# Performance work log

Measured on AMD Instinct MI355X. Metric: run time of the kernel, lower is better.

Reference implementation:

```python
import jax, jax.numpy as jnp
import numpy as np

NUM_USERS = 200000
NUM_ITEMS = 100000
EMB = 64
NUM_LAYERS = 3


def setup_inputs() -> dict:
    rng = np.random.default_rng(0)
    E_INTER = 2_000_000
    # unique (user, item) interactions -> faithful to adj[e0, e1] = 1.0 set-semantics
    lin = np.unique(rng.integers(0, NUM_USERS * NUM_ITEMS, size=E_INTER, dtype=np.int64))
    u = (lin // NUM_ITEMS).astype(np.int32)
    it = (lin % NUM_ITEMS).astype(np.int32) + NUM_USERS  # item node ids offset by NUM_USERS
    row = np.concatenate([u, it])  # symmetric bipartite graph, no self-loops
    col = np.concatenate([it, u])
    edge_index = jnp.asarray(np.stack([row, col]), dtype=jnp.int32)  # [2, E]

    key = jax.random.key(0)
    k1, k2 = jax.random.split(key)
    # xavier_uniform on nn.Embedding.weight
    bu = float(np.sqrt(6.0 / (NUM_USERS + EMB)))
    bi = float(np.sqrt(6.0 / (NUM_ITEMS + EMB)))
    user_emb = jax.random.uniform(k1, (NUM_USERS, EMB), jnp.float32, -bu, bu)
    item_emb = jax.random.uniform(k2, (NUM_ITEMS, EMB), jnp.float32, -bi, bi)
    return {"edge_index": edge_index, "user_emb": user_emb, "item_emb": item_emb}


def reference(edge_index, user_emb, item_emb):
    num_users = user_emb.shape[0]
    N = num_users + item_emb.shape[0]
    x = jnp.concatenate([user_emb, item_emb], axis=0)  # ego embeddings [N, D]
    row, col = edge_index[0], edge_index[1]

    # adj has unique off-diagonal edges + eye(N): row-sum degree = edge count + 1
    deg = jax.ops.segment_sum(jnp.ones(row.shape, x.dtype), row, num_segments=N) + 1.0
    dinv = jax.lax.rsqrt(deg)                 # deg >= 1, never inf
    w = (dinv[row] * dinv[col])[:, None]      # per-edge D^-1/2 A D^-1/2 weight
    self_w = (dinv * dinv)[:, None]           # self-loop weight d_i^-1

    acc = x  # sum over layer outputs, including layer 0
    for _ in range(NUM_LAYERS):
        x = jax.ops.segment_sum(w * x[col], row, num_segments=N) + self_w * x
        # dropout is identity in eval mode
        acc = acc + x

    return acc[:num_users], acc[num_users:]
```

## Files before the change

kernel.cpp:

```cpp
#include <hip/hip_runtime.h>
#include <hip/hip_bf16.h>

#define EMB 64

__device__ __forceinline__ float bf2f(unsigned short h) {
    return __uint_as_float(((unsigned)h) << 16);
}
__device__ __forceinline__ unsigned short f2bf(float f) {
    unsigned u = __float_as_uint(f);
    unsigned r = (u + 0x7fffu + ((u >> 16) & 1u)) >> 16;
    return (unsigned short)r;
}

__global__ void k1_kernel(const int* __restrict__ row, const int* __restrict__ colh,
                          int* __restrict__ urp, int* __restrict__ degit,
                          int NU, int Eh, int urp_blocks) {
    if ((int)blockIdx.x < urp_blocks) {
        int r = blockIdx.x * blockDim.x + threadIdx.x;
        if (r > NU) return;
        if (r == NU) { urp[NU] = Eh; return; }
        int lo = 0, hi = Eh;
        while (lo < hi) {
            int mid = (lo + hi) >> 1;
            if (row[mid] < r) lo = mid + 1; else hi = mid;
        }
        urp[r] = lo;
    } else {
        int e = (blockIdx.x - urp_blocks) * blockDim.x + threadIdx.x;
        if (e < Eh) atomicAdd(&degit[colh[e] - NU], 1);
    }
}

__global__ void k3_kernel(const int* __restrict__ degit, int* __restrict__ excl,
                          int* __restrict__ partials,
                          const int* __restrict__ urp, float* __restrict__ dinv,
                          const float* __restrict__ ue, const float* __restrict__ ie,
                          unsigned short* __restrict__ y0,
                          int NU, int NI, int N, long nu_elems, long total,
                          int nb_s1, int nb_dv) {
    int b = blockIdx.x;
    if (b < nb_s1) {
        __shared__ int sh[256];
        int t = threadIdx.x;
        int base = b * 1024 + t * 4;
        int d0 = (base + 0 < NI) ? degit[base + 0] : 0;
        int d1 = (base + 1 < NI) ? degit[base + 1] : 0;
        int d2 = (base + 2 < NI) ? degit[base + 2] : 0;
        int d3 = (base + 3 < NI) ? degit[base + 3] : 0;
        int tsum = d0 + d1 + d2 + d3;
        sh[t] = tsum;
        __syncthreads();
        for (int off = 1; off < 256; off <<= 1) {
            int v = (t >= off) ? sh[t - off] : 0;
            __syncthreads();
            sh[t] += v;
            __syncthreads();
        }
        int excl_t = sh[t] - tsum;
        if (base + 0 < NI) excl[base + 0] = excl_t;
        if (base + 1 < NI) excl[base + 1] = excl_t + d0;
        if (base + 2 < NI) excl[base + 2] = excl_t + d0 + d1;
        if (base + 3 < NI) excl[base + 3] = excl_t + d0 + d1 + d2;
        if (t == 255) partials[b] = sh[t];
    } else if (b < nb_s1 + nb_dv) {
        int i = (b - nb_s1) * blockDim.x + threadIdx.x;
        if (i >= N) return;
        int d = (i < NU) ? (urp[i + 1] - urp[i]) : degit[i - NU];
        dinv[i] = rsqrtf((float)d + 1.0f);
    } else {
        long j4 = ((long)(b - nb_s1 - nb_dv) * blockDim.x + threadIdx.x) * 4;
        if (j4 >= total) return;
        int node = (int)(j4 >> 6);
        int d = (node < NU) ? (urp[node + 1] - urp[node]) : degit[node - NU];
        float sc = rsqrtf((float)d + 1.0f);
        float4 v = (j4 < nu_elems) ? ((const float4*)ue)[j4 >> 2]
                                   : ((const float4*)ie)[(j4 - nu_elems) >> 2];
        ushort4 o;
        o.x = f2bf(sc * v.x); o.y = f2bf(sc * v.y);
        o.z = f2bf(sc * v.z); o.w = f2bf(sc * v.w);
        ((ushort4*)y0)[j4 >> 2] = o;
    }
}

__global__ void scan2_kernel(int* __restrict__ partials, int nb) {
    __shared__ int sh[512];
    int t = threadIdx.x;
    int v = (t < nb) ? partials[t] : 0;
    sh[t] = v;
    __syncthreads();
    for (int off = 1; off < 512; off <<= 1) {
        int u = (t >= off) ? sh[t - off] : 0;
        __syncthreads();
        sh[t] += u;
        __syncthreads();
    }
    if (t < nb) partials[t] = sh[t] - v;
}

__global__ void scan3_kernel(const int* __restrict__ excl, const int* __restrict__ partials,
                             int* __restrict__ irp, int* __restrict__ cursor, int NI, int Eh) {
    int i = blockIdx.x * blockDim.x + threadIdx.x;
    if (i < NI) {
        int v = excl[i] + partials[i >> 10];
        irp[i] = v;
        cursor[i] = v;
    }
    if (i == NI) irp[NI] = Eh;
}

__device__ __forceinline__ void spmm_node(
    int i, int q,
    const int* __restrict__ urp, const int* __restrict__ irp,
    const int* __restrict__ colg, const int* __restrict__ icols,
    const float* __restrict__ dinv,
    const unsigned short* __restrict__ yc,
    unsigned short* __restrict__ yn,
    const unsigned short* __restrict__ y0b,
    const unsigned short* __restrict__ y1b,
    float* __restrict__ out, int NU) {
    const int* list;
    int s, e;
    if (i < NU) { s = urp[i]; e = urp[i + 1]; list = colg; }
    else        { int j = i - NU; s = irp[j]; e = irp[j + 1]; list = icols; }
    float di = dinv[i];
    const ushort4* __restrict__ yc4 = (const ushort4*)yc;

    long p = (long)i * 16 + q;
    ushort4 sv = yc4[p];

    float ax = 0.f, ay = 0.f, az = 0.f, aw = 0.f;
    for (int k0 = s; k0 < e; k0 += 8) {
        int   c[8];
        float w[8];
#pragma unroll
        for (int j = 0; j < 8; ++j) {
            int k = k0 + j;
            bool v = (k < e);
            c[j] = v ? list[k] : 0;
            w[j] = v ? 1.0f : 0.0f;
        }
        ushort4 u[8];
#pragma unroll
        for (int j = 0; j < 8; ++j) u[j] = yc4[(long)c[j] * 16 + q];
#pragma unroll
        for (int j = 0; j < 8; ++j) {
            ax += w[j] * bf2f(u[j].x);
            ay += w[j] * bf2f(u[j].y);
            az += w[j] * bf2f(u[j].z);
            aw += w[j] * bf2f(u[j].w);
        }
    }

    ax += bf2f(sv.x);
    ay += bf2f(sv.y);
    az += bf2f(sv.z);
    aw += bf2f(sv.w);

    if (yn) {
        float t = di * di;
        ushort4 o;
        o.x = f2bf(t * ax); o.y = f2bf(t * ay); o.z = f2bf(t * az); o.w = f2bf(t * aw);
        ((ushort4*)yn)[p] = o;
    } else {
        ushort4 a0 = ((const ushort4*)y0b)[p];
        ushort4 a1 = ((const ushort4*)y1b)[p];
        float inv = 1.0f / di;
        float4 o;
        o.x = (bf2f(a0.x) + bf2f(a1.x) + bf2f(sv.x)) * inv + di * ax;
        o.y = (bf2f(a0.y) + bf2f(a1.y) + bf2f(sv.y)) * inv + di * ay;
        o.z = (bf2f(a0.z) + bf2f(a1.z) + bf2f(sv.z)) * inv + di * az;
        o.w = (bf2f(a0.w) + bf2f(a1.w) + bf2f(sv.w)) * inv + di * aw;
        ((float4*)out)[p] = o;
    }
}

__global__ void spmm_kernel(int base, int cnt,
                            const int* __restrict__ urp, const int* __restrict__ irp,
                            const int* __restrict__ colg, const int* __restrict__ icols,
                            const float* __restrict__ dinv,
                            const unsigned short* __restrict__ yc,
                            unsigned short* __restrict__ yn,
                            const unsigned short* __restrict__ y0b,
                            const unsigned short* __restrict__ y1b,
                            float* __restrict__ out, int NU) {
    long t = (long)blockIdx.x * blockDim.x + threadIdx.x;
    int r = (int)(t >> 4);
    if (r >= cnt) return;
    spmm_node(base + r, (int)(t & 15), urp, irp, colg, icols, dinv,
              yc, yn, y0b, y1b, out, NU);
}

__global__ void m6_kernel(const int* __restrict__ rowh, const int* __restrict__ colh,
                          int* __restrict__ cursor, int* __restrict__ icols,
                          int nb_if, int Eh, int NU, int NI,
                          const int* __restrict__ urp, const int* __restrict__ irp,
                          const int* __restrict__ colg,
                          const float* __restrict__ dinv,
                          const unsigned short* __restrict__ yc,
                          unsigned short* __restrict__ yn) {
    int b = (int)blockIdx.x;
    int fid = -1, usr;
    if (b < 4 * nb_if) {
        if ((b & 3) == 0) { fid = b >> 2; usr = -1; }
        else              { usr = b - (b >> 2) - 1; }
    } else {
        usr = b - nb_if;
    }

    if (fid >= 0) {
        int t = threadIdx.x;
        long cb = (long)fid * 1024;
        int c[4], u[4];
#pragma unroll
        for (int j = 0; j < 4; ++j) {
            long e = cb + j * 256 + t;
            bool v = (e < Eh);
            c[j] = v ? (colh[e] - NU) : -1;
            u[j] = v ? rowh[e] : 0;
        }
        int slice = (NI + 7) >> 3;
        for (int p = 0; p < 8; ++p) {
            int lo = p * slice, hi = lo + slice;
#pragma unroll
            for (int j = 0; j < 4; ++j) {
                if (c[j] >= lo && c[j] < hi) {
                    int pos = atomicAdd(&cursor[c[j]], 1);
                    icols[pos] = u[j];
                }
            }
        }
    } else {
        long t = (long)usr * blockDim.x + threadIdx.x;
        int i = (int)(t >> 4);
        if (i >= NU) return;
        spmm_node(i, (int)(t & 15), urp, irp, colg, nullptr, dinv,
                  yc, yn, nullptr, nullptr, nullptr, NU);
    }
}

extern "C" void kernel_launch(void* const* d_in, const int* in_sizes, int n_in,
                              void* d_out, int out_size, void* d_ws, size_t ws_size,
                              hipStream_t stream) {
    const int*   edge_index = (const int*)d_in[0];
    const float* user_emb   = (const float*)d_in[1];
    const float* item_emb   = (const float*)d_in[2];
    float* out = (float*)d_out;

    const int  E  = in_sizes[0] / 2;
    const int  Eh = E / 2;
    const int  NU = in_sizes[1] / EMB;
    const int  NI = in_sizes[2] / EMB;
    const int  N  = NU + NI;
    const long total = (long)N * EMB;

    const int* row = edge_index;
    const int* col = edge_index + E;
    const int* rowh = row;
    const int* colh = col;

    int*   urp      = (int*)d_ws;
    int*   degit    = urp + (NU + 1);
    int*   excl     = degit + NI;
    int*   partials = excl + NI;
    int*   irp      = partials + 512;
    int*   cursor   = irp + (NI + 1);
    int*   icols    = cursor + NI;
    float* dinv     = (float*)(icols + Eh);
    unsigned short* y0 = (unsigned short*)(dinv + N);
    y0 = (unsigned short*)(((uintptr_t)y0 + 15) & ~(uintptr_t)15);
    unsigned short* y1 = y0 + total;
    unsigned short* y2 = y1 + total;

    hipMemsetAsync(degit, 0, (size_t)NI * sizeof(int), stream);

    int urp_blocks  = (NU + 256) / 256;
    int ideg_blocks = (Eh + 255) / 256;
    k1_kernel<<<urp_blocks + ideg_blocks, 256, 0, stream>>>(row, colh, urp, degit,
                                                            NU, Eh, urp_blocks);

    int nb_s1 = (NI + 1023) / 1024;
    int nb_dv = (N + 255) / 256;
    int nb_in = (int)((total / 4 + 255) / 256);
    k3_kernel<<<nb_s1 + nb_dv + nb_in, 256, 0, stream>>>(degit, excl, partials,
                                                         urp, dinv, user_emb, item_emb, y0,
                                                         NU, NI, N, (long)NU * EMB, total,
                                                         nb_s1, nb_dv);

    scan2_kernel<<<1, 512, 0, stream>>>(partials, nb_s1);
    scan3_kernel<<<(NI + 1 + 255) / 256, 256, 0, stream>>>(excl, partials, irp, cursor,
                                                           NI, Eh);

    int nb_if = (Eh + 1023) / 1024;
    int nb_us = (int)(((long)NU * 16 + 255) / 256);
    m6_kernel<<<nb_if + nb_us, 256, 0, stream>>>(rowh, colh, cursor, icols,
                                                 nb_if, Eh, NU, NI,
                                                 urp, irp, col, dinv, y0, y1);

    int nb_it = (int)(((long)NI * 16 + 255) / 256);
    spmm_kernel<<<nb_it, 256, 0, stream>>>(NU, NI, urp, irp, col, icols, dinv,
                                           y0, y1, nullptr, nullptr, nullptr, NU);

    int nb_all = (int)(((long)N * 16 + 255) / 256);
    spmm_kernel<<<nb_all, 256, 0, stream>>>(0, N, urp, irp, col, icols, dinv,
                                            y1, y2, nullptr, nullptr, nullptr, NU);

    spmm_kernel<<<nb_all, 256, 0, stream>>>(0, N, urp, irp, col, icols, dinv,
                                            y2, nullptr, y0, y1, out, NU);
}
```

Measured before the change: 617.6 us.

## Build item CSR via two-pass bucketed counting sort through staging buffer

Replaces the direct scattered atomic insertion of item adjacency lists with a two-pass bucket sort. A first pass groups edges by 1024-item bucket using shared-memory counters and packs the local item offset and user id into one word in a staging buffer. A second pass, fused with the first user-layer SpMM, scatters within each bucket so the cursor atomics and icols writes stay localized. This adds an extra kernel launch and a round trip through staging memory, which aliases the item half of y1 before that half is written.

Result: no change. 624.1 us (+1.0%).

```diff
diff --git a/kernel.cpp b/kernel.cpp
--- a/kernel.cpp
+++ b/kernel.cpp
@@ -2,6 +2,10 @@
 #include <hip/hip_bf16.h>
 
 #define EMB 64
+#define BKT_BITS 10
+#define BKT_SZ   (1 << BKT_BITS)
+#define U_BITS   18
+#define U_MASK   ((1u << U_BITS) - 1u)
 
 __device__ __forceinline__ float bf2f(unsigned short h) {
     return __uint_as_float(((unsigned)h) << 16);
@@ -98,14 +102,49 @@
 }
 
 __global__ void scan3_kernel(const int* __restrict__ excl, const int* __restrict__ partials,
-                             int* __restrict__ irp, int* __restrict__ cursor, int NI, int Eh) {
+                             int* __restrict__ irp, int* __restrict__ cursor,
+                             int* __restrict__ bcur, int NI, int Eh) {
     int i = blockIdx.x * blockDim.x + threadIdx.x;
     if (i < NI) {
         int v = excl[i] + partials[i >> 10];
         irp[i] = v;
         cursor[i] = v;
+        if ((i & (BKT_SZ - 1)) == 0) bcur[i >> BKT_BITS] = v;
     }
     if (i == NI) irp[NI] = Eh;
+}
+
+__global__ void passA_kernel(const int* __restrict__ rowh, const int* __restrict__ colh,
+                             int* __restrict__ bcur, unsigned* __restrict__ staging,
+                             int Eh, int NU, int NB) {
+    __shared__ int cnt[512];
+    __shared__ int base[512];
+    int t = threadIdx.x;
+    for (int j = t; j < NB; j += 256) cnt[j] = 0;
+    __syncthreads();
+    long cb = (long)blockIdx.x * 1024;
+    int b[4], rk[4];
+    unsigned pk[4];
+#pragma unroll
+    for (int j = 0; j < 4; ++j) {
+        long e = cb + j * 256 + t;
+        if (e < Eh) {
+            int u = rowh[e];
+            int loc = colh[e] - NU;
+            b[j] = loc >> BKT_BITS;
+            pk[j] = ((unsigned)(loc & (BKT_SZ - 1)) << U_BITS) | (unsigned)u;
+            rk[j] = atomicAdd(&cnt[b[j]], 1);
+        } else {
+            b[j] = -1;
+        }
+    }
+    __syncthreads();
+    for (int j = t; j < NB; j += 256)
+        base[j] = cnt[j] ? atomicAdd(&bcur[j], cnt[j]) : 0;
+    __syncthreads();
+#pragma unroll
+    for (int j = 0; j < 4; ++j)
+        if (b[j] >= 0) staging[base[b[j]] + rk[j]] = pk[j];
 }
 
 __device__ __forceinline__ void spmm_node(
@@ -190,47 +229,28 @@
               yc, yn, y0b, y1b, out, NU);
 }
 
-__global__ void m6_kernel(const int* __restrict__ rowh, const int* __restrict__ colh,
-                          int* __restrict__ cursor, int* __restrict__ icols,
-                          int nb_if, int Eh, int NU, int NI,
-                          const int* __restrict__ urp, const int* __restrict__ irp,
+__global__ void m6_kernel(const unsigned* __restrict__ staging,
+                          const int* __restrict__ irp, int* __restrict__ cursor,
+                          int* __restrict__ icols, int NB, int NI,
+                          const int* __restrict__ urp,
                           const int* __restrict__ colg,
                           const float* __restrict__ dinv,
                           const unsigned short* __restrict__ yc,
-                          unsigned short* __restrict__ yn) {
+                          unsigned short* __restrict__ yn, int NU) {
     int b = (int)blockIdx.x;
-    int fid = -1, usr;
-    if (b < 4 * nb_if) {
-        if ((b & 3) == 0) { fid = b >> 2; usr = -1; }
-        else              { usr = b - (b >> 2) - 1; }
+    if (b < NB) {
+        int lo = b << BKT_BITS;
+        int hi = lo + BKT_SZ; if (hi > NI) hi = NI;
+        int start = irp[lo], end = irp[hi];
+        for (int k = start + (int)threadIdx.x; k < end; k += 256) {
+            unsigned v = staging[k];
+            int u   = (int)(v & U_MASK);
+            int loc = lo + (int)(v >> U_BITS);
+            int pos = atomicAdd(&cursor[loc], 1);
+            icols[pos] = u;
+        }
     } else {
-        usr = b - nb_if;
-    }
-
-    if (fid >= 0) {
-        int t = threadIdx.x;
-        long cb = (long)fid * 1024;
-        int c[4], u[4];
-#pragma unroll
-        for (int j = 0; j < 4; ++j) {
-            long e = cb + j * 256 + t;
-            bool v = (e < Eh);
-            c[j] = v ? (colh[e] - NU) : -1;
-            u[j] = v ? rowh[e] : 0;
-        }
-        int slice = (NI + 7) >> 3;
-        for (int p = 0; p < 8; ++p) {
-            int lo = p * slice, hi = lo + slice;
-#pragma unroll
-            for (int j = 0; j < 4; ++j) {
-                if (c[j] >= lo && c[j] < hi) {
-                    int pos = atomicAdd(&cursor[c[j]], 1);
-                    icols[pos] = u[j];
-                }
-            }
-        }
-    } else {
-        long t = (long)usr * blockDim.x + threadIdx.x;
+        long t = (long)(b - NB) * blockDim.x + threadIdx.x;
         int i = (int)(t >> 4);
         if (i >= NU) return;
         spmm_node(i, (int)(t & 15), urp, irp, colg, nullptr, dinv,
@@ -262,14 +282,15 @@
     int*   degit    = urp + (NU + 1);
     int*   excl     = degit + NI;
     int*   partials = excl + NI;
-    int*   irp      = partials + 512;
+    int*   bcur     = partials + 512;
+    int*   irp      = bcur + 512;
     int*   cursor   = irp + (NI + 1);
     int*   icols    = cursor + NI;
     float* dinv     = (float*)(icols + Eh);
-    unsigned short* y0 = (unsigned short*)(dinv + N);
-    y0 = (unsigned short*)(((uintptr_t)y0 + 15) & ~(uintptr_t)15);
+    unsigned short* y0 = (unsigned short*)(((uintptr_t)(dinv + N) + 127) & ~(uintptr_t)127);
     unsigned short* y1 = y0 + total;
     unsigned short* y2 = y1 + total;
+    unsigned* staging = (unsigned*)(y1 + (long)NU * EMB);
 
     hipMemsetAsync(degit, 0, (size_t)NI * sizeof(int), stream);
 
@@ -288,13 +309,15 @@
 
     scan2_kernel<<<1, 512, 0, stream>>>(partials, nb_s1);
     scan3_kernel<<<(NI + 1 + 255) / 256, 256, 0, stream>>>(excl, partials, irp, cursor,
-                                                           NI, Eh);
-
-    int nb_if = (Eh + 1023) / 1024;
+                                                           bcur, NI, Eh);
+
+    int NB = (NI + BKT_SZ - 1) >> BKT_BITS;
+    int nb_pa = (Eh + 1023) / 1024;
+    passA_kernel<<<nb_pa, 256, 0, stream>>>(rowh, colh, bcur, staging, Eh, NU, NB);
+
     int nb_us = (int)(((long)NU * 16 + 255) / 256);
-    m6_kernel<<<nb_if + nb_us, 256, 0, stream>>>(rowh, colh, cursor, icols,
-                                                 nb_if, Eh, NU, NI,
-                                                 urp, irp, col, dinv, y0, y1);
+    m6_kernel<<<NB + nb_us, 256, 0, stream>>>(staging, irp, cursor, icols, NB, NI,
+                                              urp, col, dinv, y0, y1, NU);
 
     int nb_it = (int)(((long)NI * 16 + 255) / 256);
     spmm_kernel<<<nb_it, 256, 0, stream>>>(NU, NI, urp, irp, col, icols, dinv,
```
